# Kernel tuning notes

Measured on AMD Instinct MI355X. Metric: run time of the kernel, lower is better.

The kernel has to match this reference:

```python
import jax, jax.numpy as jnp
import numpy as np

BETA = 0.5
PS = 4  # threshold rank per row, and pooling ratio N//PS


def _getM(att, ps):
    # att: [B, N]. Per-row descending sort; threshold = (ps+1)-th largest value.
    vals = -jnp.sort(-att, axis=1)            # descending sort, [B, N]
    thr = vals[:, ps, None]                   # [B, 1]
    mask = att >= thr                         # [B, N] bool
    return jnp.sum(mask.astype(att.dtype), axis=0)  # [N] counts


def setup_inputs() -> dict:
    key = jax.random.key(0)
    k1, k2, k3, k4 = jax.random.split(key, 4)
    B, N, D = 64, 2048, 512
    return {
        "x": jax.random.normal(k1, (B, N, D), dtype=jnp.float32),
        "y": jax.random.normal(k2, (B, N, N), dtype=jnp.float32),
        "attention": jax.random.normal(k3, (B, N), dtype=jnp.float32),
        "att_off": jax.random.normal(k4, (B, N), dtype=jnp.float32),
    }


def reference(x, y, attention, att_off):
    # attention is already [B, N]; flatten(start_dim=1) is a no-op here.
    M = BETA * _getM(attention, PS) + (1.0 - BETA) * _getM(att_off, PS)  # [N]
    # torch.sort(descending=True) on M; take top N//ps indices.
    top_m = jnp.argsort(-M)[: M.shape[0] // PS]  # [K], K = N//PS
    x_sel = x[:, top_m]                          # [B, K, D]
    y_sel = y[:, top_m][:, :, top_m]             # [B, K, K] (two-stage gather)
    return (x_sel, y_sel, top_m)
```

## Files before the change

kernel.cpp:

```cpp
#include <hip/hip_runtime.h>
#include <math.h>

#define NN 2048
#define BB 64
#define DD 512
#define NSEL 512

typedef float fx4 __attribute__((ext_vector_type(4)));

__device__ __forceinline__ void insert5b(float v, float t[5]) {
  float a = v, m;
  m = fmaxf(t[0], a); a = fminf(t[0], a); t[0] = m;
  m = fmaxf(t[1], a); a = fminf(t[1], a); t[1] = m;
  m = fmaxf(t[2], a); a = fminf(t[2], a); t[2] = m;
  m = fmaxf(t[3], a); a = fminf(t[3], a); t[3] = m;
  t[4] = fmaxf(t[4], a);
}

__global__ void thr_kernel(const float* __restrict__ att,
                           const float* __restrict__ aoff,
                           float* __restrict__ thr) {
  int blk  = blockIdx.x;
  const float* src = (blk < BB) ? att : aoff;
  int row  = (blk < BB) ? blk : blk - BB;
  int lane = threadIdx.x;

  float t[5] = {-INFINITY, -INFINITY, -INFINITY, -INFINITY, -INFINITY};
  const fx4* rp4 = (const fx4*)(src + (size_t)row * NN);
  #pragma unroll
  for (int k = 0; k < NN / 256; ++k) {
    fx4 v = rp4[lane + 64 * k];
    insert5b(v.x, t); insert5b(v.y, t); insert5b(v.z, t); insert5b(v.w, t);
  }

  for (int off = 1; off < 64; off <<= 1) {
    float b[5];
    #pragma unroll
    for (int k = 0; k < 5; ++k) b[k] = __shfl_xor(t[k], off, 64);
    float m[5];
    int ia = 0, ib = 0;
    #pragma unroll
    for (int k = 0; k < 5; ++k) {
      float av = t[ia], bv = b[ib];
      bool ta = (av >= bv);
      m[k] = ta ? av : bv;
      ia += ta ? 1 : 0;
      ib += ta ? 0 : 1;
    }
    #pragma unroll
    for (int k = 0; k < 5; ++k) t[k] = m[k];
  }
  if (lane == 0) thr[blk] = t[4];
}

__global__ void mkey_kernel(const float* __restrict__ att,
                            const float* __restrict__ aoff,
                            const float* __restrict__ thr,
                            int* __restrict__ key) {
  int n = blockIdx.x * 64 + threadIdx.x;
  if (n >= NN) return;
  int c = 0;
  #pragma unroll 16
  for (int b = 0; b < BB; ++b) c += (att[(size_t)b * NN + n] >= thr[b]) ? 1 : 0;
  #pragma unroll 16
  for (int b = 0; b < BB; ++b) c += (aoff[(size_t)b * NN + n] >= thr[BB + b]) ? 1 : 0;
  key[n] = c;
}

__global__ void __launch_bounds__(1024)
topm_kernel(const int* __restrict__ key,
            int* __restrict__ top_m,
            float* __restrict__ out_tail) {
  __shared__ int chist[32][132];
  __shared__ int htot[132];
  __shared__ int gbase[132];
  int t = threadIdx.x;
  int w = t >> 6, lane = t & 63;

  for (int i = t; i < 32 * 132; i += 1024) (&chist[0][0])[i] = 0;
  __syncthreads();

  int k0 = key[t];
  int k1 = key[t + 1024];
  atomicAdd(&chist[w][k0], 1);
  atomicAdd(&chist[16 + w][k1], 1);
  __syncthreads();

  {
    int c = lane & 31;
    #pragma unroll
    for (int rd = 0; rd < 5; ++rd) {
      int kb = rd * 32 + w * 2 + (lane >> 5);
      if (kb <= 128) {
        int v = chist[c][kb];
        int inc = v;
        #pragma unroll
        for (int d = 1; d < 32; d <<= 1) {
          int o = __shfl_up(inc, d, 32);
          if (c >= d) inc += o;
        }
        chist[c][kb] = inc - v;
        if (c == 31) htot[kb] = inc;
      }
    }
  }
  __syncthreads();

  if (t < 64) {
    int carry = 0;
    #pragma unroll
    for (int rd = 0; rd < 3; ++rd) {
      int k = 128 - (rd * 64 + lane);
      int v = (k >= 0) ? htot[k] : 0;
      int inc = v;
      #pragma unroll
      for (int d = 1; d < 64; d <<= 1) {
        int o = __shfl_up(inc, d, 64);
        if (lane >= d) inc += o;
      }
      if (k >= 0) gbase[k] = carry + inc - v;
      carry += __shfl(inc, 63, 64);
    }
  }
  __syncthreads();

  unsigned long long lt = (lane == 0) ? 0ull : (~0ull >> (64 - lane));
  {
    unsigned long long m = ~0ull;
    #pragma unroll
    for (int bit = 0; bit < 8; ++bit) {
      unsigned long long bb = __ballot(((k0 >> bit) & 1) != 0);
      m &= ((k0 >> bit) & 1) ? bb : ~bb;
    }
    int pre0 = __popcll(m & lt);
    int r0 = gbase[k0] + chist[w][k0] + pre0;
    if (r0 < NSEL) { top_m[r0] = t; out_tail[r0] = (float)t; }
  }
  {
    unsigned long long m = ~0ull;
    #pragma unroll
    for (int bit = 0; bit < 8; ++bit) {
      unsigned long long bb = __ballot(((k1 >> bit) & 1) != 0);
      m &= ((k1 >> bit) & 1) ? bb : ~bb;
    }
    int pre1 = __popcll(m & lt);
    int r1 = gbase[k1] + chist[16 + w][k1] + pre1;
    if (r1 < NSEL) { top_m[r1] = t + 1024; out_tail[r1] = (float)(t + 1024); }
  }
}

__global__ void __launch_bounds__(256)
gather_kernel(const float* __restrict__ x,
              const float* __restrict__ y,
              const int* __restrict__ top_m,
              float* __restrict__ xs,
              float* __restrict__ ys) {
  __shared__ float rowbuf[4][NN];
  __shared__ int cols[NSEL];
  int t = threadIdx.x;
  int w = t >> 6, lane = t & 63;
  int blk = blockIdx.x;
  int b = blk >> 4;
  int iblk = blk & 15;

  cols[t]       = top_m[t];
  cols[t + 256] = top_m[t + 256];
  __syncthreads();

  float* myrow = rowbuf[w];
  int i0 = iblk * 32 + w * 8;
  const float* ybase = y + (size_t)b * NN * NN;

  fx4 pr[8];
  {
    int r = cols[i0];
    const fx4* src = (const fx4*)(ybase + (size_t)r * NN);
    #pragma unroll
    for (int j = 0; j < 8; ++j)
      pr[j] = __builtin_nontemporal_load(&src[lane + 64 * j]);
  }

  #pragma unroll
  for (int k = 0; k < 8; ++k) {
    int i = i0 + k;
    {
      fx4* mb = (fx4*)myrow;
      #pragma unroll
      for (int j = 0; j < 8; ++j) mb[lane + 64 * j] = pr[j];
    }
    if (k < 7) {
      int rn = cols[i + 1];
      const fx4* src = (const fx4*)(ybase + (size_t)rn * NN);
      #pragma unroll
      for (int j = 0; j < 8; ++j)
        pr[j] = __builtin_nontemporal_load(&src[lane + 64 * j]);
    }
    {
      int r = cols[i];
      const fx4* xsrc = (const fx4*)(x + ((size_t)b * NN + r) * DD);
      fx4*       xdst = (fx4*)(xs + ((size_t)b * NSEL + i) * DD);
      #pragma unroll
      for (int j = 0; j < 2; ++j) {
        fx4 v = __builtin_nontemporal_load(&xsrc[lane + 64 * j]);
        __builtin_nontemporal_store(v, &xdst[lane + 64 * j]);
      }
    }
    {
      float o[8];
      #pragma unroll
      for (int j = 0; j < 8; ++j) o[j] = myrow[cols[8 * lane + j]];
      fx4* dst = (fx4*)(ys + ((size_t)b * NSEL + i) * DD);
      fx4 o0 = {o[0], o[1], o[2], o[3]};
      fx4 o1 = {o[4], o[5], o[6], o[7]};
      __builtin_nontemporal_store(o0, &dst[2 * lane]);
      __builtin_nontemporal_store(o1, &dst[2 * lane + 1]);
    }
  }
}

extern "C" void kernel_launch(void* const* d_in, const int* in_sizes, int n_in,
                              void* d_out, int out_size, void* d_ws, size_t ws_size,
                              hipStream_t stream) {
  const float* x    = (const float*)d_in[0];
  const float* y    = (const float*)d_in[1];
  const float* att  = (const float*)d_in[2];
  const float* aoff = (const float*)d_in[3];

  float* out  = (float*)d_out;
  float* xs   = out;
  float* ysel = out + (size_t)BB * NSEL * DD;
  float* tail = ysel + (size_t)BB * NSEL * NSEL;

  float* thr   = (float*)d_ws;
  int*   key   = (int*)d_ws + 128;
  int*   top_m = (int*)d_ws + 128 + NN;

  hipLaunchKernelGGL(thr_kernel, dim3(2 * BB), dim3(64), 0, stream, att, aoff, thr);
  hipLaunchKernelGGL(mkey_kernel, dim3(32), dim3(64), 0, stream, att, aoff, thr, key);
  hipLaunchKernelGGL(topm_kernel, dim3(1), dim3(1024), 0, stream, key, top_m, tail);
  hipLaunchKernelGGL(gather_kernel, dim3(BB * 16), dim3(256), 0, stream,
                     x, y, top_m, xs, ysel);
}
```

Measured before the change: 121.8 us.

## Fuse threshold, count and top-m kernels into one flag-synchronized launch

Merges the three small selection kernels into a single 161-block kernel whose block groups hand off through global atomic counters and spin-waits, instead of relying on kernel boundaries. The aim is to remove two launch gaps on the short front-end chain before the gather. The cost is an extra memset launch, spin-wait polling, and reliance on all 161 blocks being co-resident so the waits cannot deadlock. The top-m block also shrinks from 1024 to 256 threads, with each thread handling more keys.

```diff
diff --git a/kernel.cpp b/kernel.cpp
--- a/kernel.cpp
+++ b/kernel.cpp
@@ -17,135 +17,152 @@
   t[4] = fmaxf(t[4], a);
 }
 
-__global__ void thr_kernel(const float* __restrict__ att,
-                           const float* __restrict__ aoff,
-                           float* __restrict__ thr) {
-  int blk  = blockIdx.x;
-  const float* src = (blk < BB) ? att : aoff;
-  int row  = (blk < BB) ? blk : blk - BB;
-  int lane = threadIdx.x;
-
-  float t[5] = {-INFINITY, -INFINITY, -INFINITY, -INFINITY, -INFINITY};
-  const fx4* rp4 = (const fx4*)(src + (size_t)row * NN);
-  #pragma unroll
-  for (int k = 0; k < NN / 256; ++k) {
-    fx4 v = rp4[lane + 64 * k];
-    insert5b(v.x, t); insert5b(v.y, t); insert5b(v.z, t); insert5b(v.w, t);
-  }
-
-  for (int off = 1; off < 64; off <<= 1) {
-    float b[5];
-    #pragma unroll
-    for (int k = 0; k < 5; ++k) b[k] = __shfl_xor(t[k], off, 64);
-    float m[5];
-    int ia = 0, ib = 0;
-    #pragma unroll
-    for (int k = 0; k < 5; ++k) {
-      float av = t[ia], bv = b[ib];
-      bool ta = (av >= bv);
-      m[k] = ta ? av : bv;
-      ia += ta ? 1 : 0;
-      ib += ta ? 0 : 1;
-    }
-    #pragma unroll
-    for (int k = 0; k < 5; ++k) t[k] = m[k];
-  }
-  if (lane == 0) thr[blk] = t[4];
-}
-
-__global__ void mkey_kernel(const float* __restrict__ att,
-                            const float* __restrict__ aoff,
-                            const float* __restrict__ thr,
-                            int* __restrict__ key) {
-  int n = blockIdx.x * 64 + threadIdx.x;
-  if (n >= NN) return;
-  int c = 0;
-  #pragma unroll 16
-  for (int b = 0; b < BB; ++b) c += (att[(size_t)b * NN + n] >= thr[b]) ? 1 : 0;
-  #pragma unroll 16
-  for (int b = 0; b < BB; ++b) c += (aoff[(size_t)b * NN + n] >= thr[BB + b]) ? 1 : 0;
-  key[n] = c;
-}
-
-__global__ void __launch_bounds__(1024)
-topm_kernel(const int* __restrict__ key,
-            int* __restrict__ top_m,
-            float* __restrict__ out_tail) {
+__global__ void __launch_bounds__(256)
+chain_kernel(const float* __restrict__ att,
+             const float* __restrict__ aoff,
+             float* __restrict__ thr_g,
+             int* __restrict__ key_g,
+             int* __restrict__ top_m,
+             float* __restrict__ out_tail,
+             int* __restrict__ flags) {
   __shared__ int chist[32][132];
   __shared__ int htot[132];
   __shared__ int gbase[132];
-  int t = threadIdx.x;
+  int bk = blockIdx.x;
+  int t  = threadIdx.x;
   int w = t >> 6, lane = t & 63;
 
-  for (int i = t; i < 32 * 132; i += 1024) (&chist[0][0])[i] = 0;
-  __syncthreads();
-
-  int k0 = key[t];
-  int k1 = key[t + 1024];
-  atomicAdd(&chist[w][k0], 1);
-  atomicAdd(&chist[16 + w][k1], 1);
-  __syncthreads();
-
-  {
-    int c = lane & 31;
+  if (bk < 128) {
+    if (w == 0) {
+      const float* src = (bk < BB) ? att : aoff;
+      int row = (bk < BB) ? bk : bk - BB;
+      float tt[5] = {-INFINITY, -INFINITY, -INFINITY, -INFINITY, -INFINITY};
+      const fx4* rp4 = (const fx4*)(src + (size_t)row * NN);
+      #pragma unroll
+      for (int k = 0; k < NN / 256; ++k) {
+        fx4 v = rp4[lane + 64 * k];
+        insert5b(v.x, tt); insert5b(v.y, tt); insert5b(v.z, tt); insert5b(v.w, tt);
+      }
+      for (int off = 1; off < 64; off <<= 1) {
+        float bb[5];
+        #pragma unroll
+        for (int k = 0; k < 5; ++k) bb[k] = __shfl_xor(tt[k], off, 64);
+        float m[5];
+        int ia = 0, ib = 0;
+        #pragma unroll
+        for (int k = 0; k < 5; ++k) {
+          float av = tt[ia], bv = bb[ib];
+          bool ta = (av >= bv);
+          m[k] = ta ? av : bv;
+          ia += ta ? 1 : 0;
+          ib += ta ? 0 : 1;
+        }
+        #pragma unroll
+        for (int k = 0; k < 5; ++k) tt[k] = m[k];
+      }
+      if (lane == 0) thr_g[bk] = tt[4];
+    }
+    __syncthreads();
+    __threadfence();
+    if (t == 0) atomicAdd(&flags[0], 1);
+
+  } else if (bk < 160) {
+    if (t == 0) {
+      while (__hip_atomic_load(&flags[0], __ATOMIC_ACQUIRE,
+                               __HIP_MEMORY_SCOPE_AGENT) < 128) { }
+    }
+    __syncthreads();
+    __threadfence();
+    if (w == 0) {
+      int n = (bk - 128) * 64 + lane;
+      int c = 0;
+      #pragma unroll 16
+      for (int b = 0; b < BB; ++b) c += (att[(size_t)b * NN + n] >= thr_g[b]) ? 1 : 0;
+      #pragma unroll 16
+      for (int b = 0; b < BB; ++b) c += (aoff[(size_t)b * NN + n] >= thr_g[BB + b]) ? 1 : 0;
+      key_g[n] = c;
+    }
+    __syncthreads();
+    __threadfence();
+    if (t == 0) atomicAdd(&flags[1], 1);
+
+  } else {
+    if (t == 0) {
+      while (__hip_atomic_load(&flags[1], __ATOMIC_ACQUIRE,
+                               __HIP_MEMORY_SCOPE_AGENT) < 32) { }
+    }
+    __syncthreads();
+    __threadfence();
+
+    for (int i = t; i < 32 * 132; i += 256) (&chist[0][0])[i] = 0;
+    __syncthreads();
+
+    unsigned long long lt = (lane == 0) ? 0ull : (~0ull >> (64 - lane));
+    int kk[8];
+    int pre[8];
     #pragma unroll
-    for (int rd = 0; rd < 5; ++rd) {
-      int kb = rd * 32 + w * 2 + (lane >> 5);
-      if (kb <= 128) {
-        int v = chist[c][kb];
+    for (int p = 0; p < 8; ++p) {
+      int c = w * 8 + p;
+      int n = c * 64 + lane;
+      int k = key_g[n];
+      kk[p] = k;
+      atomicAdd(&chist[c][k], 1);
+      unsigned long long m = ~0ull;
+      #pragma unroll
+      for (int bit = 0; bit < 8; ++bit) {
+        unsigned long long bb = __ballot(((k >> bit) & 1) != 0);
+        m &= ((k >> bit) & 1) ? bb : ~bb;
+      }
+      pre[p] = __popcll(m & lt);
+    }
+    __syncthreads();
+
+    {
+      int c = lane & 31;
+      #pragma unroll
+      for (int rd = 0; rd < 17; ++rd) {
+        int kb = rd * 8 + w * 2 + (lane >> 5);
+        if (kb <= 128) {
+          int v = chist[c][kb];
+          int inc = v;
+          #pragma unroll
+          for (int d = 1; d < 32; d <<= 1) {
+            int o = __shfl_up(inc, d, 32);
+            if (c >= d) inc += o;
+          }
+          chist[c][kb] = inc - v;
+          if (c == 31) htot[kb] = inc;
+        }
+      }
+    }
+    __syncthreads();
+
+    if (t < 64) {
+      int carry = 0;
+      #pragma unroll
+      for (int rd = 0; rd < 3; ++rd) {
+        int k = 128 - (rd * 64 + lane);
+        int v = (k >= 0) ? htot[k] : 0;
         int inc = v;
         #pragma unroll
-        for (int d = 1; d < 32; d <<= 1) {
-          int o = __shfl_up(inc, d, 32);
-          if (c >= d) inc += o;
+        for (int d = 1; d < 64; d <<= 1) {
+          int o = __shfl_up(inc, d, 64);
+          if (lane >= d) inc += o;
         }
-        chist[c][kb] = inc - v;
-        if (c == 31) htot[kb] = inc;
-      }
-    }
-  }
-  __syncthreads();
-
-  if (t < 64) {
-    int carry = 0;
+        if (k >= 0) gbase[k] = carry + inc - v;
+        carry += __shfl(inc, 63, 64);
+      }
+    }
+    __syncthreads();
+
     #pragma unroll
-    for (int rd = 0; rd < 3; ++rd) {
-      int k = 128 - (rd * 64 + lane);
-      int v = (k >= 0) ? htot[k] : 0;
-      int inc = v;
-      #pragma unroll
-      for (int d = 1; d < 64; d <<= 1) {
-        int o = __shfl_up(inc, d, 64);
-        if (lane >= d) inc += o;
-      }
-      if (k >= 0) gbase[k] = carry + inc - v;
-      carry += __shfl(inc, 63, 64);
-    }
-  }
-  __syncthreads();
-
-  unsigned long long lt = (lane == 0) ? 0ull : (~0ull >> (64 - lane));
-  {
-    unsigned long long m = ~0ull;
-    #pragma unroll
-    for (int bit = 0; bit < 8; ++bit) {
-      unsigned long long bb = __ballot(((k0 >> bit) & 1) != 0);
-      m &= ((k0 >> bit) & 1) ? bb : ~bb;
-    }
-    int pre0 = __popcll(m & lt);
-    int r0 = gbase[k0] + chist[w][k0] + pre0;
-    if (r0 < NSEL) { top_m[r0] = t; out_tail[r0] = (float)t; }
-  }
-  {
-    unsigned long long m = ~0ull;
-    #pragma unroll
-    for (int bit = 0; bit < 8; ++bit) {
-      unsigned long long bb = __ballot(((k1 >> bit) & 1) != 0);
-      m &= ((k1 >> bit) & 1) ? bb : ~bb;
-    }
-    int pre1 = __popcll(m & lt);
-    int r1 = gbase[k1] + chist[16 + w][k1] + pre1;
-    if (r1 < NSEL) { top_m[r1] = t + 1024; out_tail[r1] = (float)(t + 1024); }
+    for (int p = 0; p < 8; ++p) {
+      int c = w * 8 + p;
+      int n = c * 64 + lane;
+      int k = kk[p];
+      int r = gbase[k] + chist[c][k] + pre[p];
+      if (r < NSEL) { top_m[r] = n; out_tail[r] = (float)n; }
+    }
   }
 }
 
@@ -231,13 +248,14 @@
   float* ysel = out + (size_t)BB * NSEL * DD;
   float* tail = ysel + (size_t)BB * NSEL * NSEL;
 
-  float* thr   = (float*)d_ws;
-  int*   key   = (int*)d_ws + 128;
+  float* thr_g = (float*)d_ws;
+  int*   key_g = (int*)d_ws + 128;
   int*   top_m = (int*)d_ws + 128 + NN;
-
-  hipLaunchKernelGGL(thr_kernel, dim3(2 * BB), dim3(64), 0, stream, att, aoff, thr);
-  hipLaunchKernelGGL(mkey_kernel, dim3(32), dim3(64), 0, stream, att, aoff, thr, key);
-  hipLaunchKernelGGL(topm_kernel, dim3(1), dim3(1024), 0, stream, key, top_m, tail);
+  int*   flags = (int*)d_ws + 128 + NN + NSEL;
+
+  hipMemsetAsync(flags, 0, 2 * sizeof(int), stream);
+  hipLaunchKernelGGL(chain_kernel, dim3(161), dim3(256), 0, stream,
+                     att, aoff, thr_g, key_g, top_m, tail, flags);
   hipLaunchKernelGGL(gather_kernel, dim3(BB * 16), dim3(256), 0, stream,
                      x, y, top_m, xs, ysel);
 }
```

Result: slower. 141.1 us (+15.8%).
